# Kernel tuning notes

Hardware: AMD Instinct MI355X
Metric: run time of the kernel (lower is better)

Reference implementation:

```python
import jax, jax.numpy as jnp
import numpy as np

NUM_SAMPLE = 64
MIN_DEPTH, MAX_DEPTH = 10.0, 40.0


def setup_inputs() -> dict:
    key = jax.random.key(0)
    k1, k2 = jax.random.split(key)
    B, C, H, W = 2, 3, 256, 320
    left_img = jax.random.normal(k1, (B, C, H, W), dtype=jnp.float32)
    right_img = jax.random.normal(k2, (B, C, H, W), dtype=jnp.float32)
    # Realistic pinhole projections: P = [[K@R, K@t],[0,0,0,1]], R=I, t=(tx,0,0)
    fx = fy = 320.0
    K = np.array([[fx, 0.0, W / 2.0], [0.0, fy, H / 2.0], [0.0, 0.0, 1.0]], dtype=np.float32)
    def make_proj(tx):
        P = np.eye(4, dtype=np.float32)
        P[:3, :3] = K
        P[:3, 3] = K @ np.array([tx, 0.0, 0.0], dtype=np.float32)
        return P
    left_proj = jnp.asarray(np.tile(make_proj(0.1)[None], (B, 1, 1)))
    right_proj = jnp.asarray(np.tile(make_proj(-0.1)[None], (B, 1, 1)))
    gt_proj = jnp.asarray(np.tile(make_proj(0.0)[None], (B, 1, 1)))
    return {"left_img": left_img, "right_img": right_img, "left_proj": left_proj,
            "right_proj": right_proj, "gt_proj": gt_proj}


def _bilinear_sample_zeros(img, x, y):
    """grid_sample(bilinear, zeros padding, align_corners=True) at pixel coords.
    img: [B,C,H,W]; x,y: [B,N]. Returns [B,C,N]."""
    B, C, H, W = img.shape
    x0 = jnp.floor(x)
    y0 = jnp.floor(y)
    wx1 = x - x0
    wy1 = y - y0
    img_flat = img.reshape(B, C, H * W)
    def corner(xc, yc, w):
        valid = (xc >= 0) & (xc <= W - 1) & (yc >= 0) & (yc <= H - 1)
        xi = jnp.clip(xc, 0, W - 1).astype(jnp.int32)
        yi = jnp.clip(yc, 0, H - 1).astype(jnp.int32)
        flat = (yi * W + xi)[:, None, :]  # [B,1,N]
        vals = jnp.take_along_axis(img_flat, jnp.broadcast_to(flat, (B, C, flat.shape[2])), axis=2)
        return vals * (w * valid)[:, None, :]
    return (corner(x0, y0, (1 - wx1) * (1 - wy1))
            + corner(x0 + 1, y0, wx1 * (1 - wy1))
            + corner(x0, y0 + 1, (1 - wx1) * wy1)
            + corner(x0 + 1, y0 + 1, wx1 * wy1))


def _warp(src_img, src_proj, ref_proj, depth):
    """Plane-sweep projective warp of src into the ref view at each depth.
    src_img: [B,C,H,W]; depth: [B,D,H,W] -> [B,C,D,H,W]."""
    B, C, H, W = src_img.shape
    D = depth.shape[1]
    proj = src_proj @ jnp.linalg.inv(ref_proj)  # [B,4,4]
    rot, trans = proj[:, :3, :3], proj[:, :3, 3]
    ys, xs = jnp.meshgrid(jnp.arange(H, dtype=src_img.dtype), jnp.arange(W, dtype=src_img.dtype), indexing="ij")
    xyz = jnp.stack([xs.ravel(), ys.ravel(), jnp.ones(H * W, dtype=src_img.dtype)])  # [3,HW]
    rot_xyz = jnp.einsum("bij,jn->bin", rot, xyz)  # [B,3,HW]
    pxyz = rot_xyz[:, :, None, :] * depth.reshape(B, 1, D, H * W) + trans[:, :, None, None]  # [B,3,D,HW]
    neg = pxyz[:, 2] <= 1e-3  # guard against points behind camera
    z = jnp.where(neg, 1.0, pxyz[:, 2])
    px = jnp.where(neg, float(W), pxyz[:, 0]) / z
    py = jnp.where(neg, float(H), pxyz[:, 1]) / z
    warped = _bilinear_sample_zeros(src_img, px.reshape(B, -1), py.reshape(B, -1))
    return warped.reshape(B, C, D, H, W)


def reference(left_img, right_img, left_proj, right_proj, gt_proj):
    B, C, H, W = left_img.shape
    inv_min, inv_max = 1.0 / MIN_DEPTH, 1.0 / MAX_DEPTH
    # depth_sample == None branch: stratified uniform inverse-depth sampling
    noise = jax.random.uniform(jax.random.key(1), (B, NUM_SAMPLE, H, W), dtype=left_img.dtype)
    s = noise + jnp.arange(NUM_SAMPLE, dtype=left_img.dtype)[None, :, None, None]
    depth = 1.0 / (inv_max + s / NUM_SAMPLE * (inv_min - inv_max))  # [B,D,H,W]
    warped_left = _warp(left_img, left_proj, gt_proj, depth)
    warped_right = _warp(right_img, right_proj, gt_proj, depth)
    return jnp.sum(jnp.abs(warped_right - warped_left), axis=1)  # [B,D,H,W]
```

## Files before the change

### kernel.cpp

```cpp
#include <hip/hip_runtime.h>
#include <stdint.h>

#define W_ 320
#define H_ 256
#define HW_ (W_ * H_)
#define NS_ 64
#define B_ 2
#define HALF_ (NS_ * HW_)
#define D_PER 4


__device__ void inv4(const float* m, float* invOut) {
    float a[4][8];
    for (int i = 0; i < 4; i++) {
        for (int j = 0; j < 4; j++) {
            a[i][j] = m[i * 4 + j];
            a[i][j + 4] = (i == j) ? 1.0f : 0.0f;
        }
    }
    for (int c = 0; c < 4; c++) {
        int p = c;
        float best = fabsf(a[c][c]);
        for (int r = c + 1; r < 4; r++) {
            float v = fabsf(a[r][c]);
            if (v > best) { best = v; p = r; }
        }
        if (p != c) {
            for (int j = 0; j < 8; j++) { float tmp = a[c][j]; a[c][j] = a[p][j]; a[p][j] = tmp; }
        }
        float pinv = 1.0f / a[c][c];
        for (int j = 0; j < 8; j++) a[c][j] *= pinv;
        for (int r = 0; r < 4; r++) {
            if (r == c) continue;
            float f = a[r][c];
            for (int j = 0; j < 8; j++) a[r][j] -= f * a[c][j];
        }
    }
    for (int i = 0; i < 4; i++)
        for (int j = 0; j < 4; j++) invOut[i * 4 + j] = a[i][j + 4];
}


__global__ __launch_bounds__(256) void prepass_kernel(const float* __restrict__ limg,
                                                      const float* __restrict__ rimg,
                                                      const float* __restrict__ lproj,
                                                      const float* __restrict__ rproj,
                                                      const float* __restrict__ gproj,
                                                      float* __restrict__ pd,
                                                      float4* __restrict__ out4) {
    int p = blockIdx.x * 256 + threadIdx.x;

    if (p < 4) {
        int b = p >> 1;
        int s = p & 1;
        float inv[16];
        inv4(gproj + b * 16, inv);
        const float* sp = (s == 0 ? lproj : rproj) + b * 16;
        float* o = pd + p * 12;
        for (int i = 0; i < 3; i++) {
            for (int j = 0; j < 3; j++) {
                float acc = 0.0f;
                for (int k = 0; k < 4; k++) acc += sp[i * 4 + k] * inv[k * 4 + j];
                o[i * 3 + j] = acc;
            }
        }
        for (int i = 0; i < 3; i++) {
            float acc = 0.0f;
            for (int k = 0; k < 4; k++) acc += sp[i * 4 + k] * inv[k * 4 + 3];
            o[9 + i] = acc;
        }
        const float eps = 1e-4f;
        bool ok = fabsf(o[0] - 1.0f) < eps && fabsf(o[1]) < eps && fabsf(o[2]) < eps &&
                  fabsf(o[3]) < eps && fabsf(o[4] - 1.0f) < eps && fabsf(o[5]) < eps &&
                  fabsf(o[6]) < eps && fabsf(o[7]) < eps && fabsf(o[8] - 1.0f) < eps &&
                  fabsf(o[10]) < eps && fabsf(o[11]) < eps;
        pd[48 + p] = ok ? 1.0f : 0.0f;
    }

    if (p < B_ * HW_) {
        int b = p / HW_;
        int pix = p - b * HW_;
        const float* Lb = limg + b * 3 * HW_;
        const float* Rb = rimg + b * 3 * HW_;
        out4[p] = make_float4(Lb[pix], Lb[HW_ + pix], Lb[2 * HW_ + pix], 0.0f);
        out4[B_ * HW_ + p] = make_float4(Rb[pix], Rb[HW_ + pix], Rb[2 * HW_ + pix], 0.0f);
    }
}


__device__ __forceinline__ float u01(uint32_t b) {
    b = (b >> 9) | 0x3F800000u;
    return __uint_as_float(b) - 1.0f;
}

#define TF_ROUND(r) { x0 += x1; x1 = (x1 << (r)) | (x1 >> (32 - (r))); x1 ^= x0; }

__device__ __forceinline__ uint32_t threefry20_xor(uint32_t c0, uint32_t c1) {
    const uint32_t ks0 = 0u, ks1 = 1u, ks2 = 0x1BD11BDAu ^ ks0 ^ ks1;
    uint32_t x0 = c0 + ks0;
    uint32_t x1 = c1 + ks1;
    TF_ROUND(13) TF_ROUND(15) TF_ROUND(26) TF_ROUND(6)
    x0 += ks1; x1 += ks2 + 1u;
    TF_ROUND(17) TF_ROUND(29) TF_ROUND(16) TF_ROUND(24)
    x0 += ks2; x1 += ks0 + 2u;
    TF_ROUND(13) TF_ROUND(15) TF_ROUND(26) TF_ROUND(6)
    x0 += ks0; x1 += ks1 + 3u;
    TF_ROUND(17) TF_ROUND(29) TF_ROUND(16) TF_ROUND(24)
    x0 += ks1; x1 += ks2 + 4u;
    TF_ROUND(13) TF_ROUND(15) TF_ROUND(26) TF_ROUND(6)
    x0 += ks2; x1 += ks0 + 5u;
    return x0 ^ x1;
}


struct F3 { float x, y, z; };

__device__ __forceinline__ F3 lerp1d(const float4* __restrict__ row, float px) {
    float x0f = floorf(px);
    float wx1 = px - x0f;
    float wx0 = 1.0f - wx1;
    int xi = (int)x0f;
    bool v0 = (unsigned)xi < (unsigned)W_;
    bool v1 = (unsigned)(xi + 1) < (unsigned)W_;
    int c0 = min(max(xi, 0), W_ - 1);
    int c1 = min(max(xi + 1, 0), W_ - 1);
    float w0 = v0 ? wx0 : 0.0f;
    float w1 = v1 ? wx1 : 0.0f;
    float4 p0 = row[c0];
    float4 p1 = row[c1];
    F3 o;
    o.x = p0.x * w0 + p1.x * w1;
    o.y = p0.y * w0 + p1.y * w1;
    o.z = p0.z * w0 + p1.z * w1;
    return o;
}

__device__ __forceinline__ F3 bil4(const float4* __restrict__ img, float px, float py) {
    float x0f = floorf(px), y0f = floorf(py);
    float wx1 = px - x0f, wy1 = py - y0f;
    float wx0 = 1.0f - wx1, wy0 = 1.0f - wy1;
    int xi = (int)x0f, yi = (int)y0f;
    bool vx0 = (unsigned)xi < (unsigned)W_;
    bool vx1 = (unsigned)(xi + 1) < (unsigned)W_;
    bool vy0 = (unsigned)yi < (unsigned)H_;
    bool vy1 = (unsigned)(yi + 1) < (unsigned)H_;
    int cx0 = min(max(xi, 0), W_ - 1);
    int cx1 = min(max(xi + 1, 0), W_ - 1);
    int r0 = min(max(yi, 0), H_ - 1) * W_;
    int r1 = min(max(yi + 1, 0), H_ - 1) * W_;
    float w00 = (vx0 && vy0) ? wx0 * wy0 : 0.0f;
    float w10 = (vx1 && vy0) ? wx1 * wy0 : 0.0f;
    float w01 = (vx0 && vy1) ? wx0 * wy1 : 0.0f;
    float w11 = (vx1 && vy1) ? wx1 * wy1 : 0.0f;
    float4 p00 = img[r0 + cx0];
    float4 p10 = img[r0 + cx1];
    float4 p01 = img[r1 + cx0];
    float4 p11 = img[r1 + cx1];
    F3 o;
    o.x = p00.x * w00 + p10.x * w10 + p01.x * w01 + p11.x * w11;
    o.y = p00.y * w00 + p10.y * w10 + p01.y * w01 + p11.y * w11;
    o.z = p00.z * w00 + p10.z * w10 + p01.z * w01 + p11.z * w11;
    return o;
}

__device__ __forceinline__ F3 proj_bil(const float4* __restrict__ img,
                                       float rx, float ry, float rz,
                                       float tx, float ty, float tz, float depth) {
    float px_ = rx * depth + tx;
    float py_ = ry * depth + ty;
    float pz_ = rz * depth + tz;
    bool neg = pz_ <= 0.001f;
    float z = neg ? 1.0f : pz_;
    float zi = __builtin_amdgcn_rcpf(z);
    float px = (neg ? (float)W_ : px_) * zi;
    float py = (neg ? (float)H_ : py_) * zi;
    return bil4(img, px, py);
}

__device__ __forceinline__ float adiff3(F3 a, F3 b) {
    return fabsf(a.x - b.x) + fabsf(a.y - b.y) + fabsf(a.z - b.z);
}


__global__ __launch_bounds__(256) void volume4_kernel(const float4* __restrict__ img4,
                                                      const float* __restrict__ pd,
                                                      float* __restrict__ out) {
    int u = blockIdx.x * 256 + threadIdx.x;
    if (u >= HALF_ / D_PER) return;
    int pix = u % HW_;
    int dgrp = u / HW_;
    int w = pix % W_;
    int h = pix / W_;
    float fx = (float)w;

    bool fast = (pd[48] != 0.0f) & (pd[49] != 0.0f) & (pd[50] != 0.0f) & (pd[51] != 0.0f);

    const float4* L0 = img4;
    const float4* L1 = img4 + HW_;
    const float4* R0 = img4 + 2 * HW_;
    const float4* R1 = img4 + 3 * HW_;

    if (fast) {
        float tl0 = pd[0 * 12 + 9];
        float tr0 = pd[1 * 12 + 9];
        float tl1 = pd[2 * 12 + 9];
        float tr1 = pd[3 * 12 + 9];
        const float4* rowL0 = L0 + h * W_;
        const float4* rowR0 = R0 + h * W_;
        const float4* rowL1 = L1 + h * W_;
        const float4* rowR1 = R1 + h * W_;

#pragma unroll
        for (int j = 0; j < D_PER; j++) {
            int d = dgrp * D_PER + j;
            int t = d * HW_ + pix;
            uint32_t bits0 = threefry20_xor(0u, (uint32_t)t);
            uint32_t bits1 = threefry20_xor(0u, (uint32_t)(t + HALF_));
            float fd = (float)d;
            float den0 = 0.025f + (u01(bits0) + fd) * 0.001171875f;
            float den1 = 0.025f + (u01(bits1) + fd) * 0.001171875f;

            F3 l0 = lerp1d(rowL0, fmaf(tl0, den0, fx));
            F3 r0 = lerp1d(rowR0, fmaf(tr0, den0, fx));
            F3 l1 = lerp1d(rowL1, fmaf(tl1, den1, fx));
            F3 r1 = lerp1d(rowR1, fmaf(tr1, den1, fx));

            out[t] = adiff3(r0, l0);
            out[t + HALF_] = adiff3(r1, l1);
        }
    } else {
        float fy = (float)h;
        float rx[4], ry[4], rz[4], tx[4], ty[4], tz[4];
#pragma unroll
        for (int s = 0; s < 4; s++) {
            const float* q = pd + s * 12;
            rx[s] = q[0] * fx + q[1] * fy + q[2];
            ry[s] = q[3] * fx + q[4] * fy + q[5];
            rz[s] = q[6] * fx + q[7] * fy + q[8];
            tx[s] = q[9]; ty[s] = q[10]; tz[s] = q[11];
        }
#pragma unroll
        for (int j = 0; j < D_PER; j++) {
            int d = dgrp * D_PER + j;
            int t = d * HW_ + pix;
            uint32_t bits0 = threefry20_xor(0u, (uint32_t)t);
            uint32_t bits1 = threefry20_xor(0u, (uint32_t)(t + HALF_));
            float fd = (float)d;
            float s0 = u01(bits0) + fd;
            float s1 = u01(bits1) + fd;
            float depth0 = __builtin_amdgcn_rcpf(0.025f + (s0 * 0.015625f) * 0.075f);
            float depth1 = __builtin_amdgcn_rcpf(0.025f + (s1 * 0.015625f) * 0.075f);

            F3 l0 = proj_bil(L0, rx[0], ry[0], rz[0], tx[0], ty[0], tz[0], depth0);
            F3 r0 = proj_bil(R0, rx[1], ry[1], rz[1], tx[1], ty[1], tz[1], depth0);
            F3 l1 = proj_bil(L1, rx[2], ry[2], rz[2], tx[2], ty[2], tz[2], depth1);
            F3 r1 = proj_bil(R1, rx[3], ry[3], rz[3], tx[3], ty[3], tz[3], depth1);

            out[t] = adiff3(r0, l0);
            out[t + HALF_] = adiff3(r1, l1);
        }
    }
}


__device__ __forceinline__ void corner(const float* __restrict__ img, float xc, float yc, float wgt,
                                       float& c0, float& c1, float& c2) {
    bool valid = (xc >= 0.0f) & (xc <= (float)(W_ - 1)) & (yc >= 0.0f) & (yc <= (float)(H_ - 1));
    float xcc = fminf(fmaxf(xc, 0.0f), (float)(W_ - 1));
    float ycc = fminf(fmaxf(yc, 0.0f), (float)(H_ - 1));
    int xi = (int)xcc;
    int yi = (int)ycc;
    int off = yi * W_ + xi;
    float wv = valid ? wgt : 0.0f;
    c0 += img[off] * wv;
    c1 += img[HW_ + off] * wv;
    c2 += img[2 * HW_ + off] * wv;
}

__device__ __forceinline__ void proj_sample_s(const float* __restrict__ img, const float* __restrict__ pd,
                                              float depth, float x, float y,
                                              float& c0, float& c1, float& c2) {
    float rx = pd[0] * x + pd[1] * y + pd[2];
    float ry = pd[3] * x + pd[4] * y + pd[5];
    float rz = pd[6] * x + pd[7] * y + pd[8];
    float px_ = rx * depth + pd[9];
    float py_ = ry * depth + pd[10];
    float pz_ = rz * depth + pd[11];
    bool neg = pz_ <= 0.001f;
    float z = neg ? 1.0f : pz_;
    float zi = __builtin_amdgcn_rcpf(z);
    float px = (neg ? (float)W_ : px_) * zi;
    float py = (neg ? (float)H_ : py_) * zi;
    float x0f = floorf(px), y0f = floorf(py);
    float wx1 = px - x0f, wy1 = py - y0f;
    float wx0 = 1.0f - wx1, wy0 = 1.0f - wy1;
    c0 = 0.0f; c1 = 0.0f; c2 = 0.0f;
    corner(img, x0f,        y0f,        wx0 * wy0, c0, c1, c2);
    corner(img, x0f + 1.0f, y0f,        wx1 * wy0, c0, c1, c2);
    corner(img, x0f,        y0f + 1.0f, wx0 * wy1, c0, c1, c2);
    corner(img, x0f + 1.0f, y0f + 1.0f, wx1 * wy1, c0, c1, c2);
}

__global__ __launch_bounds__(256) void volume_kernel(const float* __restrict__ limg,
                                                     const float* __restrict__ rimg,
                                                     const float* __restrict__ pd,
                                                     float* __restrict__ out) {
    int t = blockIdx.x * 256 + threadIdx.x;
    if (t >= HALF_) return;
    uint32_t bits0 = threefry20_xor(0u, (uint32_t)t);
    uint32_t bits1 = threefry20_xor(0u, (uint32_t)t + (uint32_t)HALF_);
    float n0 = u01(bits0);
    float n1 = u01(bits1);
    int w = t % W_;
    int rest = t / W_;
    int h = rest % H_;
    int d = rest / H_;
    float fd = (float)d;
    float depth0 = __builtin_amdgcn_rcpf(0.025f + ((n0 + fd) * 0.015625f) * 0.075f);
    float depth1 = __builtin_amdgcn_rcpf(0.025f + ((n1 + fd) * 0.015625f) * 0.075f);
    float fx = (float)w;
    float fy = (float)h;
    float l0, l1, l2, r0, r1, r2;
    proj_sample_s(limg, pd + 0, depth0, fx, fy, l0, l1, l2);
    proj_sample_s(rimg, pd + 12, depth0, fx, fy, r0, r1, r2);
    out[t] = fabsf(r0 - l0) + fabsf(r1 - l1) + fabsf(r2 - l2);
    proj_sample_s(limg + 3 * HW_, pd + 24, depth1, fx, fy, l0, l1, l2);
    proj_sample_s(rimg + 3 * HW_, pd + 36, depth1, fx, fy, r0, r1, r2);
    out[t + HALF_] = fabsf(r0 - l0) + fabsf(r1 - l1) + fabsf(r2 - l2);
}

__global__ void setup_only_kernel(const float* __restrict__ lproj, const float* __restrict__ rproj,
                                  const float* __restrict__ gproj, float* __restrict__ pd) {
    int tid = threadIdx.x;
    if (tid >= 4) return;
    int b = tid >> 1;
    int s = tid & 1;
    float inv[16];
    inv4(gproj + b * 16, inv);
    const float* sp = (s == 0 ? lproj : rproj) + b * 16;
    float* o = pd + tid * 12;
    for (int i = 0; i < 3; i++)
        for (int j = 0; j < 3; j++) {
            float acc = 0.0f;
            for (int k = 0; k < 4; k++) acc += sp[i * 4 + k] * inv[k * 4 + j];
            o[i * 3 + j] = acc;
        }
    for (int i = 0; i < 3; i++) {
        float acc = 0.0f;
        for (int k = 0; k < 4; k++) acc += sp[i * 4 + k] * inv[k * 4 + 3];
        o[9 + i] = acc;
    }
}

extern "C" void kernel_launch(void* const* d_in, const int* in_sizes, int n_in,
                              void* d_out, int out_size, void* d_ws, size_t ws_size,
                              hipStream_t stream) {
    const float* limg  = (const float*)d_in[0];
    const float* rimg  = (const float*)d_in[1];
    const float* lproj = (const float*)d_in[2];
    const float* rproj = (const float*)d_in[3];
    const float* gproj = (const float*)d_in[4];
    float* out = (float*)d_out;
    float* pd  = (float*)d_ws;
    float4* img4 = (float4*)((char*)d_ws + 256);

    const size_t need = 256 + (size_t)4 * HW_ * sizeof(float4);

    if (ws_size >= need) {
        prepass_kernel<<<(B_ * HW_ + 255) / 256, 256, 0, stream>>>(limg, rimg, lproj, rproj, gproj, pd, img4);
        volume4_kernel<<<(HALF_ / D_PER + 255) / 256, 256, 0, stream>>>(img4, pd, out);
    } else {
        setup_only_kernel<<<1, 64, 0, stream>>>(lproj, rproj, gproj, pd);
        volume_kernel<<<HALF_ / 256, 256, 0, stream>>>(limg, rimg, pd, out);
    }
}
```

Before: 102.6 us.

## Share three row texels across four consecutive depth samples in fast path

In the rectified fast path, each thread now computes the horizontal disparity for all four of its depth samples, takes the floor of the minimum, and loads only three adjacent row pixels. Each depth's lerp then picks from those three, where before each depth loaded its own two. This relies on the four disparities spanning under one pixel, which is why the fast-path check now also bounds the translation. It cuts gathers from 8 to 3 per image per thread at the cost of extra selects. The three-texel window is exact only while the disparity spread within a depth group stays below one pixel.

```diff
diff --git a/kernel.cpp b/kernel.cpp
--- a/kernel.cpp
+++ b/kernel.cpp
@@ -73,7 +73,8 @@
         bool ok = fabsf(o[0] - 1.0f) < eps && fabsf(o[1]) < eps && fabsf(o[2]) < eps &&
                   fabsf(o[3]) < eps && fabsf(o[4] - 1.0f) < eps && fabsf(o[5]) < eps &&
                   fabsf(o[6]) < eps && fabsf(o[7]) < eps && fabsf(o[8] - 1.0f) < eps &&
-                  fabsf(o[10]) < eps && fabsf(o[11]) < eps;
+                  fabsf(o[10]) < eps && fabsf(o[11]) < eps &&
+                  fabsf(o[9]) < 160.0f;
         pd[48 + p] = ok ? 1.0f : 0.0f;
     }
 
@@ -115,24 +116,48 @@
 
 struct F3 { float x, y, z; };
 
-__device__ __forceinline__ F3 lerp1d(const float4* __restrict__ row, float px) {
-    float x0f = floorf(px);
-    float wx1 = px - x0f;
-    float wx0 = 1.0f - wx1;
-    int xi = (int)x0f;
-    bool v0 = (unsigned)xi < (unsigned)W_;
-    bool v1 = (unsigned)(xi + 1) < (unsigned)W_;
-    int c0 = min(max(xi, 0), W_ - 1);
-    int c1 = min(max(xi + 1, 0), W_ - 1);
-    float w0 = v0 ? wx0 : 0.0f;
-    float w1 = v1 ? wx1 : 0.0f;
-    float4 p0 = row[c0];
-    float4 p1 = row[c1];
-    F3 o;
-    o.x = p0.x * w0 + p1.x * w1;
-    o.y = p0.y * w0 + p1.y * w1;
-    o.z = p0.z * w0 + p1.z * w1;
-    return o;
+__device__ __forceinline__ float adiff3(F3 a, F3 b) {
+    return fabsf(a.x - b.x) + fabsf(a.y - b.y) + fabsf(a.z - b.z);
+}
+
+__device__ __forceinline__ void row_sample4(const float4* __restrict__ row, float t0,
+                                            const float den[D_PER], int w, F3 res[D_PER]) {
+    float disp[D_PER];
+#pragma unroll
+    for (int j = 0; j < D_PER; j++) disp[j] = t0 * den[j];
+    float m = fminf(fminf(disp[0], disp[1]), fminf(disp[2], disp[3]));
+    float fm = floorf(m);
+    int X = w + (int)fm;
+
+    F3 q[3];
+#pragma unroll
+    for (int k = 0; k < 3; k++) {
+        int xk = X + k;
+        bool v = (unsigned)xk < (unsigned)W_;
+        int c = min(max(xk, 0), W_ - 1);
+        float4 pv = row[c];
+        q[k].x = v ? pv.x : 0.0f;
+        q[k].y = v ? pv.y : 0.0f;
+        q[k].z = v ? pv.z : 0.0f;
+    }
+
+#pragma unroll
+    for (int j = 0; j < D_PER; j++) {
+        float fdj = floorf(disp[j]);
+        float wx1 = disp[j] - fdj;
+        float wx0 = 1.0f - wx1;
+        bool hi = fdj > fm;
+        F3 p0, p1;
+        p0.x = hi ? q[1].x : q[0].x;
+        p0.y = hi ? q[1].y : q[0].y;
+        p0.z = hi ? q[1].z : q[0].z;
+        p1.x = hi ? q[2].x : q[1].x;
+        p1.y = hi ? q[2].y : q[1].y;
+        p1.z = hi ? q[2].z : q[1].z;
+        res[j].x = p0.x * wx0 + p1.x * wx1;
+        res[j].y = p0.y * wx0 + p1.y * wx1;
+        res[j].z = p0.z * wx0 + p1.z * wx1;
+    }
 }
 
 __device__ __forceinline__ F3 bil4(const float4* __restrict__ img, float px, float py) {
@@ -177,10 +202,6 @@
     return bil4(img, px, py);
 }
 
-__device__ __forceinline__ float adiff3(F3 a, F3 b) {
-    return fabsf(a.x - b.x) + fabsf(a.y - b.y) + fabsf(a.z - b.z);
-}
-
 
 __global__ __launch_bounds__(256) void volume4_kernel(const float4* __restrict__ img4,
                                                       const float* __restrict__ pd,
@@ -191,7 +212,6 @@
     int dgrp = u / HW_;
     int w = pix % W_;
     int h = pix / W_;
-    float fx = (float)w;
 
     bool fast = (pd[48] != 0.0f) & (pd[49] != 0.0f) & (pd[50] != 0.0f) & (pd[51] != 0.0f);
 
@@ -199,6 +219,8 @@
     const float4* L1 = img4 + HW_;
     const float4* R0 = img4 + 2 * HW_;
     const float4* R1 = img4 + 3 * HW_;
+
+    int tbase = dgrp * D_PER * HW_ + pix;
 
     if (fast) {
         float tl0 = pd[0 * 12 + 9];
@@ -210,25 +232,32 @@
         const float4* rowL1 = L1 + h * W_;
         const float4* rowR1 = R1 + h * W_;
 
+        float den0[D_PER], den1[D_PER];
 #pragma unroll
         for (int j = 0; j < D_PER; j++) {
             int d = dgrp * D_PER + j;
-            int t = d * HW_ + pix;
+            int t = tbase + j * HW_;
             uint32_t bits0 = threefry20_xor(0u, (uint32_t)t);
             uint32_t bits1 = threefry20_xor(0u, (uint32_t)(t + HALF_));
             float fd = (float)d;
-            float den0 = 0.025f + (u01(bits0) + fd) * 0.001171875f;
-            float den1 = 0.025f + (u01(bits1) + fd) * 0.001171875f;
-
-            F3 l0 = lerp1d(rowL0, fmaf(tl0, den0, fx));
-            F3 r0 = lerp1d(rowR0, fmaf(tr0, den0, fx));
-            F3 l1 = lerp1d(rowL1, fmaf(tl1, den1, fx));
-            F3 r1 = lerp1d(rowR1, fmaf(tr1, den1, fx));
-
-            out[t] = adiff3(r0, l0);
-            out[t + HALF_] = adiff3(r1, l1);
-        }
+            den0[j] = 0.025f + (u01(bits0) + fd) * 0.001171875f;
+            den1[j] = 0.025f + (u01(bits1) + fd) * 0.001171875f;
+        }
+
+        F3 l[D_PER], r[D_PER];
+        row_sample4(rowL0, tl0, den0, w, l);
+        row_sample4(rowR0, tr0, den0, w, r);
+#pragma unroll
+        for (int j = 0; j < D_PER; j++)
+            out[tbase + j * HW_] = adiff3(r[j], l[j]);
+
+        row_sample4(rowL1, tl1, den1, w, l);
+        row_sample4(rowR1, tr1, den1, w, r);
+#pragma unroll
+        for (int j = 0; j < D_PER; j++)
+            out[tbase + j * HW_ + HALF_] = adiff3(r[j], l[j]);
     } else {
+        float fx = (float)w;
         float fy = (float)h;
         float rx[4], ry[4], rz[4], tx[4], ty[4], tz[4];
 #pragma unroll
@@ -242,7 +271,7 @@
 #pragma unroll
         for (int j = 0; j < D_PER; j++) {
             int d = dgrp * D_PER + j;
-            int t = d * HW_ + pix;
+            int t = tbase + j * HW_;
             uint32_t bits0 = threefry20_xor(0u, (uint32_t)t);
             uint32_t bits1 = threefry20_xor(0u, (uint32_t)(t + HALF_));
             float fd = (float)d;
```

New measurement: 101.2 us. About the same (-1.4%).

## Pad image rows and reuse three-texel window across eight depths per thread

Applied to the files above, without the earlier changes.

The prepass now writes the images as zero-padded rows of stride 352 with a 16-texel offset, so out-of-range horizontal taps read zeros and need no validity checks. Each thread now covers eight depth samples instead of four. In the rectified fast path it loads one fixed three-texel window per image and interpolates every depth with hat weights, replacing two gathers per depth. This assumes the disparity spread across eight consecutive depths stays within one texel, guarded by an extra check on the translation magnitude. The window is chosen from the sign of the translation and the end depths, and the risk is wrong results if the disparity range is larger than the padding or the window covers.

```diff
diff --git a/kernel.cpp b/kernel.cpp
--- a/kernel.cpp
+++ b/kernel.cpp
@@ -7,7 +7,10 @@
 #define NS_ 64
 #define B_ 2
 #define HALF_ (NS_ * HW_)
-#define D_PER 4
+#define D_PER 8
+#define PSTRIDE 352
+#define POFF 16
+#define PIMG (256 * PSTRIDE)
 
 
 __device__ void inv4(const float* m, float* invOut) {
@@ -73,17 +76,27 @@
         bool ok = fabsf(o[0] - 1.0f) < eps && fabsf(o[1]) < eps && fabsf(o[2]) < eps &&
                   fabsf(o[3]) < eps && fabsf(o[4] - 1.0f) < eps && fabsf(o[5]) < eps &&
                   fabsf(o[6]) < eps && fabsf(o[7]) < eps && fabsf(o[8] - 1.0f) < eps &&
-                  fabsf(o[10]) < eps && fabsf(o[11]) < eps;
+                  fabsf(o[10]) < eps && fabsf(o[11]) < eps &&
+                  fabsf(o[9]) < 100.0f;
         pd[48 + p] = ok ? 1.0f : 0.0f;
     }
 
-    if (p < B_ * HW_) {
-        int b = p / HW_;
-        int pix = p - b * HW_;
-        const float* Lb = limg + b * 3 * HW_;
-        const float* Rb = rimg + b * 3 * HW_;
-        out4[p] = make_float4(Lb[pix], Lb[HW_ + pix], Lb[2 * HW_ + pix], 0.0f);
-        out4[B_ * HW_ + p] = make_float4(Rb[pix], Rb[HW_ + pix], Rb[2 * HW_ + pix], 0.0f);
+    if (p < 4 * PIMG) {
+        int img = p / PIMG;
+        int rem = p - img * PIMG;
+        int h = rem / PSTRIDE;
+        int xp = rem - h * PSTRIDE;
+        int x = xp - POFF;
+        bool v = (unsigned)x < (unsigned)W_;
+        int b = img & 1;
+        const float* src = (img < 2 ? limg : rimg) + b * 3 * HW_;
+        int pix = h * W_ + min(max(x, 0), W_ - 1);
+        float4 val;
+        val.x = v ? src[pix] : 0.0f;
+        val.y = v ? src[HW_ + pix] : 0.0f;
+        val.z = v ? src[2 * HW_ + pix] : 0.0f;
+        val.w = 0.0f;
+        out4[p] = val;
     }
 }
 
@@ -112,26 +125,26 @@
     return x0 ^ x1;
 }
 
+__device__ __forceinline__ float noise_den(uint32_t t, float fd) {
+    return 0.025f + (u01(threefry20_xor(0u, t)) + fd) * 0.001171875f;
+}
+
 
 struct F3 { float x, y, z; };
 
-__device__ __forceinline__ F3 lerp1d(const float4* __restrict__ row, float px) {
-    float x0f = floorf(px);
-    float wx1 = px - x0f;
-    float wx0 = 1.0f - wx1;
-    int xi = (int)x0f;
-    bool v0 = (unsigned)xi < (unsigned)W_;
-    bool v1 = (unsigned)(xi + 1) < (unsigned)W_;
-    int c0 = min(max(xi, 0), W_ - 1);
-    int c1 = min(max(xi + 1, 0), W_ - 1);
-    float w0 = v0 ? wx0 : 0.0f;
-    float w1 = v1 ? wx1 : 0.0f;
-    float4 p0 = row[c0];
-    float4 p1 = row[c1];
+__device__ __forceinline__ float adiff3(F3 a, F3 b) {
+    return fabsf(a.x - b.x) + fabsf(a.y - b.y) + fabsf(a.z - b.z);
+}
+
+__device__ __forceinline__ F3 hat3(float4 q0, float4 q1, float4 q2, float x) {
+    float t = x - 1.0f;
+    float w0 = fmaxf(0.0f, 1.0f - x);
+    float w1 = 1.0f - fabsf(t);
+    float w2 = fmaxf(0.0f, t);
     F3 o;
-    o.x = p0.x * w0 + p1.x * w1;
-    o.y = p0.y * w0 + p1.y * w1;
-    o.z = p0.z * w0 + p1.z * w1;
+    o.x = q0.x * w0 + q1.x * w1 + q2.x * w2;
+    o.y = q0.y * w0 + q1.y * w1 + q2.y * w2;
+    o.z = q0.z * w0 + q1.z * w1 + q2.z * w2;
     return o;
 }
 
@@ -144,10 +157,10 @@
     bool vx1 = (unsigned)(xi + 1) < (unsigned)W_;
     bool vy0 = (unsigned)yi < (unsigned)H_;
     bool vy1 = (unsigned)(yi + 1) < (unsigned)H_;
-    int cx0 = min(max(xi, 0), W_ - 1);
-    int cx1 = min(max(xi + 1, 0), W_ - 1);
-    int r0 = min(max(yi, 0), H_ - 1) * W_;
-    int r1 = min(max(yi + 1, 0), H_ - 1) * W_;
+    int cx0 = min(max(xi, 0), W_ - 1) + POFF;
+    int cx1 = min(max(xi + 1, 0), W_ - 1) + POFF;
+    int r0 = min(max(yi, 0), H_ - 1) * PSTRIDE;
+    int r1 = min(max(yi + 1, 0), H_ - 1) * PSTRIDE;
     float w00 = (vx0 && vy0) ? wx0 * wy0 : 0.0f;
     float w10 = (vx1 && vy0) ? wx1 * wy0 : 0.0f;
     float w01 = (vx0 && vy1) ? wx0 * wy1 : 0.0f;
@@ -177,12 +190,8 @@
     return bil4(img, px, py);
 }
 
-__device__ __forceinline__ float adiff3(F3 a, F3 b) {
-    return fabsf(a.x - b.x) + fabsf(a.y - b.y) + fabsf(a.z - b.z);
-}
-
-
-__global__ __launch_bounds__(256) void volume4_kernel(const float4* __restrict__ img4,
+
+__global__ __launch_bounds__(256) void volume8_kernel(const float4* __restrict__ img4,
                                                       const float* __restrict__ pd,
                                                       float* __restrict__ out) {
     int u = blockIdx.x * 256 + threadIdx.x;
@@ -191,44 +200,62 @@
     int dgrp = u / HW_;
     int w = pix % W_;
     int h = pix / W_;
-    float fx = (float)w;
+    int d0 = dgrp * D_PER;
+    int tbase = d0 * HW_ + pix;
 
     bool fast = (pd[48] != 0.0f) & (pd[49] != 0.0f) & (pd[50] != 0.0f) & (pd[51] != 0.0f);
 
-    const float4* L0 = img4;
-    const float4* L1 = img4 + HW_;
-    const float4* R0 = img4 + 2 * HW_;
-    const float4* R1 = img4 + 3 * HW_;
+    const float4* rowL0 = img4 + 0 * PIMG + h * PSTRIDE + POFF + w;
+    const float4* rowL1 = img4 + 1 * PIMG + h * PSTRIDE + POFF + w;
+    const float4* rowR0 = img4 + 2 * PIMG + h * PSTRIDE + POFF + w;
+    const float4* rowR1 = img4 + 3 * PIMG + h * PSTRIDE + POFF + w;
 
     if (fast) {
         float tl0 = pd[0 * 12 + 9];
         float tr0 = pd[1 * 12 + 9];
         float tl1 = pd[2 * 12 + 9];
         float tr1 = pd[3 * 12 + 9];
-        const float4* rowL0 = L0 + h * W_;
-        const float4* rowR0 = R0 + h * W_;
-        const float4* rowL1 = L1 + h * W_;
-        const float4* rowR1 = R1 + h * W_;
+
+        float den0[D_PER], den1[D_PER];
+        den0[0]         = noise_den((uint32_t)tbase,                          (float)d0);
+        den0[D_PER - 1] = noise_den((uint32_t)(tbase + (D_PER - 1) * HW_),    (float)(d0 + D_PER - 1));
+        den1[0]         = noise_den((uint32_t)(tbase + HALF_),                (float)d0);
+        den1[D_PER - 1] = noise_den((uint32_t)(tbase + (D_PER - 1) * HW_ + HALF_), (float)(d0 + D_PER - 1));
+
+        float dmL0 = (tl0 >= 0.0f) ? den0[0] : den0[D_PER - 1];
+        float dmR0 = (tr0 >= 0.0f) ? den0[0] : den0[D_PER - 1];
+        float dmL1 = (tl1 >= 0.0f) ? den1[0] : den1[D_PER - 1];
+        float dmR1 = (tr1 >= 0.0f) ? den1[0] : den1[D_PER - 1];
+        float fmL0 = floorf(tl0 * dmL0);
+        float fmR0 = floorf(tr0 * dmR0);
+        float fmL1 = floorf(tl1 * dmL1);
+        float fmR1 = floorf(tr1 * dmR1);
+        const float4* tL0 = rowL0 + (int)fmL0;
+        const float4* tR0 = rowR0 + (int)fmR0;
+        const float4* tL1 = rowL1 + (int)fmL1;
+        const float4* tR1 = rowR1 + (int)fmR1;
+        float4 qL0a = tL0[0], qL0b = tL0[1], qL0c = tL0[2];
+        float4 qR0a = tR0[0], qR0b = tR0[1], qR0c = tR0[2];
+        float4 qL1a = tL1[0], qL1b = tL1[1], qL1c = tL1[2];
+        float4 qR1a = tR1[0], qR1b = tR1[1], qR1c = tR1[2];
+
+#pragma unroll
+        for (int j = 1; j < D_PER - 1; j++) {
+            den0[j] = noise_den((uint32_t)(tbase + j * HW_),         (float)(d0 + j));
+            den1[j] = noise_den((uint32_t)(tbase + j * HW_ + HALF_), (float)(d0 + j));
+        }
 
 #pragma unroll
         for (int j = 0; j < D_PER; j++) {
-            int d = dgrp * D_PER + j;
-            int t = d * HW_ + pix;
-            uint32_t bits0 = threefry20_xor(0u, (uint32_t)t);
-            uint32_t bits1 = threefry20_xor(0u, (uint32_t)(t + HALF_));
-            float fd = (float)d;
-            float den0 = 0.025f + (u01(bits0) + fd) * 0.001171875f;
-            float den1 = 0.025f + (u01(bits1) + fd) * 0.001171875f;
-
-            F3 l0 = lerp1d(rowL0, fmaf(tl0, den0, fx));
-            F3 r0 = lerp1d(rowR0, fmaf(tr0, den0, fx));
-            F3 l1 = lerp1d(rowL1, fmaf(tl1, den1, fx));
-            F3 r1 = lerp1d(rowR1, fmaf(tr1, den1, fx));
-
-            out[t] = adiff3(r0, l0);
-            out[t + HALF_] = adiff3(r1, l1);
+            F3 l0 = hat3(qL0a, qL0b, qL0c, tl0 * den0[j] - fmL0);
+            F3 r0 = hat3(qR0a, qR0b, qR0c, tr0 * den0[j] - fmR0);
+            out[tbase + j * HW_] = adiff3(r0, l0);
+            F3 l1 = hat3(qL1a, qL1b, qL1c, tl1 * den1[j] - fmL1);
+            F3 r1 = hat3(qR1a, qR1b, qR1c, tr1 * den1[j] - fmR1);
+            out[tbase + j * HW_ + HALF_] = adiff3(r1, l1);
         }
     } else {
+        float fx = (float)w;
         float fy = (float)h;
         float rx[4], ry[4], rz[4], tx[4], ty[4], tz[4];
 #pragma unroll
@@ -239,22 +266,24 @@
             rz[s] = q[6] * fx + q[7] * fy + q[8];
             tx[s] = q[9]; ty[s] = q[10]; tz[s] = q[11];
         }
+        const float4* I0 = img4;
+        const float4* I1 = img4 + PIMG;
+        const float4* I2 = img4 + 2 * PIMG;
+        const float4* I3 = img4 + 3 * PIMG;
 #pragma unroll
         for (int j = 0; j < D_PER; j++) {
-            int d = dgrp * D_PER + j;
-            int t = d * HW_ + pix;
+            int d = d0 + j;
+            int t = tbase + j * HW_;
             uint32_t bits0 = threefry20_xor(0u, (uint32_t)t);
             uint32_t bits1 = threefry20_xor(0u, (uint32_t)(t + HALF_));
             float fd = (float)d;
-            float s0 = u01(bits0) + fd;
-            float s1 = u01(bits1) + fd;
-            float depth0 = __builtin_amdgcn_rcpf(0.025f + (s0 * 0.015625f) * 0.075f);
-            float depth1 = __builtin_amdgcn_rcpf(0.025f + (s1 * 0.015625f) * 0.075f);
-
-            F3 l0 = proj_bil(L0, rx[0], ry[0], rz[0], tx[0], ty[0], tz[0], depth0);
-            F3 r0 = proj_bil(R0, rx[1], ry[1], rz[1], tx[1], ty[1], tz[1], depth0);
-            F3 l1 = proj_bil(L1, rx[2], ry[2], rz[2], tx[2], ty[2], tz[2], depth1);
-            F3 r1 = proj_bil(R1, rx[3], ry[3], rz[3], tx[3], ty[3], tz[3], depth1);
+            float depth0 = __builtin_amdgcn_rcpf(0.025f + (u01(bits0) + fd) * 0.001171875f);
+            float depth1 = __builtin_amdgcn_rcpf(0.025f + (u01(bits1) + fd) * 0.001171875f);
+
+            F3 l0 = proj_bil(I0, rx[0], ry[0], rz[0], tx[0], ty[0], tz[0], depth0);
+            F3 r0 = proj_bil(I2, rx[1], ry[1], rz[1], tx[1], ty[1], tz[1], depth0);
+            F3 l1 = proj_bil(I1, rx[2], ry[2], rz[2], tx[2], ty[2], tz[2], depth1);
+            F3 r1 = proj_bil(I3, rx[3], ry[3], rz[3], tx[3], ty[3], tz[3], depth1);
 
             out[t] = adiff3(r0, l0);
             out[t + HALF_] = adiff3(r1, l1);
@@ -364,11 +393,11 @@
     float* pd  = (float*)d_ws;
     float4* img4 = (float4*)((char*)d_ws + 256);
 
-    const size_t need = 256 + (size_t)4 * HW_ * sizeof(float4);
+    const size_t need = 256 + (size_t)4 * PIMG * sizeof(float4);
 
     if (ws_size >= need) {
-        prepass_kernel<<<(B_ * HW_ + 255) / 256, 256, 0, stream>>>(limg, rimg, lproj, rproj, gproj, pd, img4);
-        volume4_kernel<<<(HALF_ / D_PER + 255) / 256, 256, 0, stream>>>(img4, pd, out);
+        prepass_kernel<<<(4 * PIMG + 255) / 256, 256, 0, stream>>>(limg, rimg, lproj, rproj, gproj, pd, img4);
+        volume8_kernel<<<(HALF_ / D_PER + 255) / 256, 256, 0, stream>>>(img4, pd, out);
     } else {
         setup_only_kernel<<<1, 64, 0, stream>>>(lproj, rproj, gproj, pd);
         volume_kernel<<<HALF_ / 256, 256, 0, stream>>>(limg, rimg, pd, out);
```

Result: faster. 99.91 us (-2.7%).
